# Performance work log

Measured on AMD Instinct MI355X. Metric: run time of the kernel, lower is better.

Reference implementation:

```python
import jax, jax.numpy as jnp
import numpy as np

N, E = 50000, 800000
IN_DIM, HID, OUT_DIM, H = 64, 64, 32, 2
NEG_SLOPE = 0.2
TEMP = 1.0
EPS = 1e-20


def gat_conv(x, edge_index, W, att_src, att_dst, bias):
    """PyG GATConv (concat=True, add_self_loops=True, eval mode so dropout off)."""
    n = x.shape[0]
    C = att_src.shape[1]
    # add self-loops (PyG default)
    loops = jnp.arange(n, dtype=edge_index.dtype)
    src = jnp.concatenate([edge_index[0], loops])
    dst = jnp.concatenate([edge_index[1], loops])
    xl = (x @ W).reshape(n, H, C)                      # [N,H,C]
    a_src = (xl * att_src[None]).sum(-1)               # [N,H]
    a_dst = (xl * att_dst[None]).sum(-1)               # [N,H]
    alpha = jax.nn.leaky_relu(a_src[src] + a_dst[dst], NEG_SLOPE)  # [E',H]
    amax = jax.ops.segment_max(alpha, dst, num_segments=n)
    alpha = jnp.exp(alpha - amax[dst])
    denom = jax.ops.segment_sum(alpha, dst, num_segments=n)
    alpha = alpha / (denom[dst] + 1e-16)
    msg = xl[src] * alpha[..., None]                   # [E',H,C]
    out = jax.ops.segment_sum(msg, dst, num_segments=n)
    return out.reshape(n, H * C) + bias


def setup_inputs() -> dict:
    key = jax.random.key(0)
    ks = jax.random.split(key, 18)
    s = 0.05
    inp = {
        'x': jax.random.normal(ks[0], (N, IN_DIM), jnp.float32),
        'edge_index': jax.random.randint(ks[1], (2, E), 0, N, jnp.int64
                                         if jax.config.jax_enable_x64 else jnp.int32).astype(jnp.int32),
        'W0': jax.random.normal(ks[2], (IN_DIM, H * HID)) * s,
        'att_src0': jax.random.normal(ks[3], (H, HID)) * s,
        'att_dst0': jax.random.normal(ks[4], (H, HID)) * s,
        'bias0': jax.random.normal(ks[5], (H * HID,)) * s,
        'fcw0': jax.random.normal(ks[6], (H * HID, HID)) * s,
        'fcb0': jax.random.normal(ks[7], (HID,)) * s,
        'W1': jax.random.normal(ks[8], (HID, H * HID)) * s,
        'att_src1': jax.random.normal(ks[9], (H, HID)) * s,
        'att_dst1': jax.random.normal(ks[10], (H, HID)) * s,
        'bias1': jax.random.normal(ks[11], (H * HID,)) * s,
        'fcw1': jax.random.normal(ks[12], (H * HID, HID)) * s,
        'fcb1': jax.random.normal(ks[13], (HID,)) * s,
        'out_w': jax.random.normal(ks[14], (HID, OUT_DIM)) * s,
        'out_b': jax.random.normal(ks[15], (OUT_DIM,)) * s,
        'gumbel_u': jax.random.uniform(ks[16], (N, OUT_DIM), jnp.float32),
    }
    return inp


def reference(x, edge_index, W0, att_src0, att_dst0, bias0, fcw0, fcb0,
              W1, att_src1, att_dst1, bias1, fcw1, fcb1, out_w, out_b, gumbel_u):
    h = gat_conv(x, edge_index, W0, att_src0, att_dst0, bias0)
    h = jax.nn.elu(h) @ fcw0 + fcb0
    h = gat_conv(h, edge_index, W1, att_src1, att_dst1, bias1)
    h = jax.nn.elu(h) @ fcw1 + fcb1
    logits = h @ out_w + out_b
    g = -jnp.log(-jnp.log(gumbel_u + EPS) + EPS)
    return jax.nn.softmax((logits + g) / TEMP, axis=-1)
```

## Files before the change

### kernel.cpp

```cpp
#include <hip/hip_runtime.h>
#include <hip/hip_fp16.h>
#include <math.h>

#define HEADS 2
#define FDIM 128
#define INDIM 64
#define ODIM 32
#define NEG_SLOPE 0.2f
#define BSH 7
#define BW  128
#define NBLK 128

typedef _Float16 f16x8 __attribute__((ext_vector_type(8)));
typedef float f32x4 __attribute__((ext_vector_type(4)));
union H8 { uint4 u; f16x8 v; __half2 h2[4]; };
union H4 { uint2 u; __half2 h2[2]; };

__device__ __forceinline__ float elu1(float v) { return v > 0.f ? v : __expf(v) - 1.f; }

#define MFMA16(a, b, c) __builtin_amdgcn_mfma_f32_16x16x32_f16((a), (b), (c), 0, 0, 0)

__global__ __launch_bounds__(256) void k_hist2(const int* __restrict__ ei, int E_,
                                               int* __restrict__ cnt, int nb, int epb) {
    __shared__ int h[512];
    int t = threadIdx.x, blk = blockIdx.x;
    for (int i = t; i < nb; i += 256) h[i] = 0;
    __syncthreads();
    int e0 = blk * epb, e1 = min(E_, e0 + epb);
    for (int e = e0 + t; e < e1; e += 256)
        atomicAdd(&h[ei[E_ + e] >> BSH], 1);
    __syncthreads();
    for (int i = t; i < nb; i += 256) cnt[i * NBLK + blk] = h[i];
}

__global__ __launch_bounds__(512) void k_scanb(const int* __restrict__ cnt,
                                               int* __restrict__ bstart,
                                               int* __restrict__ base, int nb, int E_) {
    __shared__ int sc[512];
    int t = threadIdx.x;
    int tot = 0;
    if (t < nb)
        for (int k = 0; k < NBLK; ++k) tot += cnt[t * NBLK + k];
    sc[t] = tot;
    __syncthreads();
    for (int o = 1; o < 512; o <<= 1) {
        int add = (t >= o) ? sc[t - o] : 0;
        __syncthreads();
        sc[t] += add;
        __syncthreads();
    }
    int ex = sc[t] - tot;
    if (t < nb) {
        bstart[t] = ex;
        int run = ex;
        for (int k = 0; k < NBLK; ++k) {
            base[t * NBLK + k] = run;
            run += cnt[t * NBLK + k];
        }
    }
    if (t == 0) bstart[nb] = E_;
}

__global__ __launch_bounds__(256) void k_scatter2(const int* __restrict__ ei, int E_,
                                                  const int* __restrict__ base,
                                                  unsigned* __restrict__ ebuf,
                                                  int nb, int epb) {
    __shared__ int pcur[512];
    int t = threadIdx.x, blk = blockIdx.x;
    for (int i = t; i < nb; i += 256) pcur[i] = base[i * NBLK + blk];
    __syncthreads();
    int e0 = blk * epb, e1 = min(E_, e0 + epb);
    for (int e = e0 + t; e < e1; e += 256) {
        int s = ei[e], d = ei[E_ + e];
        int slot = atomicAdd(&pcur[d >> BSH], 1);
        ebuf[slot] = ((unsigned)(d & (BW - 1)) << 25) | (unsigned)s;
    }
}

__global__ __launch_bounds__(256) void k_bfill(const unsigned* __restrict__ ebuf,
                                               const int* __restrict__ bstart,
                                               int* __restrict__ offs,
                                               int* __restrict__ csr_src, int n) {
    __shared__ int hist[BW], sc[BW], pcur[BW];
    int b = blockIdx.x;
    int t = threadIdx.x;
    int base_ = bstart[b];
    int cnt = bstart[b + 1] - base_;
    int d0 = b << BSH;
    if (t < BW) hist[t] = 0;
    __syncthreads();
    for (int i = t; i < cnt; i += 256)
        atomicAdd(&hist[ebuf[base_ + i] >> 25], 1);
    __syncthreads();
    int v = (t < BW) ? hist[t] : 0;
    if (t < BW) sc[t] = v;
    __syncthreads();
    for (int o = 1; o < BW; o <<= 1) {
        int add = (t < BW && t >= o) ? sc[t - o] : 0;
        __syncthreads();
        if (t < BW) sc[t] += add;
        __syncthreads();
    }
    if (t < BW) {
        int abspos = base_ + sc[t] - v;
        pcur[t] = abspos;
        if (d0 + t < n) offs[d0 + t] = abspos;
    }
    __syncthreads();
    for (int i = t; i < cnt; i += 256) {
        unsigned u = ebuf[base_ + i];
        int slot = atomicAdd(&pcur[u >> 25], 1);
        csr_src[slot] = (int)(u & 0x1FFFFFFu);
    }
}

__global__ __launch_bounds__(128) void k_fuse_w(
    const float* __restrict__ W0,
    const float* __restrict__ fcw0, const float* __restrict__ fcb0, const float* __restrict__ W1,
    const float* __restrict__ fcw1, const float* __restrict__ fcb1,
    const float* __restrict__ out_w, const float* __restrict__ out_b,
    __half* __restrict__ W0T, __half* __restrict__ WfT, float* __restrict__ bf,
    __half* __restrict__ WfoT, float* __restrict__ bfo)
{
    int b = blockIdx.x, c = threadIdx.x;
    if (b < 128) {
        float acc = 0.f;
        for (int j = 0; j < 64; ++j) acc = fmaf(fcw0[b * 64 + j], W1[j * 128 + c], acc);
        WfT[c * 128 + b] = __float2half(acc);
    } else if (b == 128) {
        float acc = 0.f;
        for (int j = 0; j < 64; ++j) acc = fmaf(fcb0[j], W1[j * 128 + c], acc);
        bf[c] = acc;
    } else if (b < 257) {
        int k = b - 129;
        if (c < 32) {
            float acc = 0.f;
            for (int j = 0; j < 64; ++j) acc = fmaf(fcw1[k * 64 + j], out_w[j * 32 + c], acc);
            WfoT[c * 128 + k] = __float2half(acc);
        }
    } else if (b == 257) {
        if (c < 32) {
            float acc = 0.f;
            for (int j = 0; j < 64; ++j) acc = fmaf(fcb1[j], out_w[j * 32 + c], acc);
            bfo[c] = acc + out_b[c];
        }
    } else {
        int k = b - 258;
        W0T[c * 64 + k] = __float2half(W0[k * 128 + c]);
    }
}

__global__ __launch_bounds__(256, 2) void k_mm_att1(
    const float* __restrict__ x, const __half* __restrict__ w0t,
    const float* __restrict__ att_src, const float* __restrict__ att_dst,
    __half* __restrict__ xl, float* __restrict__ a_src, float* __restrict__ a_dst,
    int n, int ntiles, int nwaves)
{
    int lane = threadIdx.x & 63;
    int wid = blockIdx.x * 4 + (threadIdx.x >> 6);
    int m = lane & 15, q = lane >> 4;

    H8 A[8][2];
    #pragma unroll
    for (int nt = 0; nt < 8; ++nt)
        #pragma unroll
        for (int kt = 0; kt < 2; ++kt)
            A[nt][kt].u = *(const uint4*)(w0t + (size_t)(nt * 16 + m) * 64 + kt * 32 + q * 8);

    for (int t = wid; t < ntiles; t += nwaves) {
        int rb = t * 16;
        int row = rb + m; if (row >= n) row = n - 1;
        H8 B[2];
        #pragma unroll
        for (int kt = 0; kt < 2; ++kt) {
            const float4* p = (const float4*)(x + (size_t)row * 64 + kt * 32 + q * 8);
            float4 p0 = p[0], p1 = p[1];
            B[kt].h2[0] = __floats2half2_rn(p0.x, p0.y);
            B[kt].h2[1] = __floats2half2_rn(p0.z, p0.w);
            B[kt].h2[2] = __floats2half2_rn(p1.x, p1.y);
            B[kt].h2[3] = __floats2half2_rn(p1.z, p1.w);
        }
        f32x4 acc[8];
        #pragma unroll
        for (int nt = 0; nt < 8; ++nt) {
            acc[nt] = {0.f, 0.f, 0.f, 0.f};
            acc[nt] = MFMA16(A[nt][0].v, B[0].v, acc[nt]);
            acc[nt] = MFMA16(A[nt][1].v, B[1].v, acc[nt]);
        }
        float ps0 = 0.f, ps1 = 0.f, pd0 = 0.f, pd1 = 0.f;
        bool ok = (rb + m) < n;
        #pragma unroll
        for (int nt = 0; nt < 8; ++nt) {
            float4 asv = *(const float4*)(att_src + nt * 16 + q * 4);
            float4 adv = *(const float4*)(att_dst + nt * 16 + q * 4);
            f32x4 d = acc[nt];
            H4 pk;
            pk.h2[0] = __floats2half2_rn(d[0], d[1]);
            pk.h2[1] = __floats2half2_rn(d[2], d[3]);
            if (ok) *(uint2*)(xl + (size_t)(rb + m) * 128 + nt * 16 + q * 4) = pk.u;
            float cs = d[0] * asv.x + d[1] * asv.y + d[2] * asv.z + d[3] * asv.w;
            float cd = d[0] * adv.x + d[1] * adv.y + d[2] * adv.z + d[3] * adv.w;
            if (nt < 4) { ps0 += cs; pd0 += cd; } else { ps1 += cs; pd1 += cd; }
        }
        ps0 += __shfl_xor(ps0, 16, 64); ps0 += __shfl_xor(ps0, 32, 64);
        ps1 += __shfl_xor(ps1, 16, 64); ps1 += __shfl_xor(ps1, 32, 64);
        pd0 += __shfl_xor(pd0, 16, 64); pd0 += __shfl_xor(pd0, 32, 64);
        pd1 += __shfl_xor(pd1, 16, 64); pd1 += __shfl_xor(pd1, 32, 64);
        if (lane < 16 && ok) {
            *(float2*)(a_src + (size_t)(rb + m) * 2) = make_float2(ps0, ps1);
            *(float2*)(a_dst + (size_t)(rb + m) * 2) = make_float2(pd0, pd1);
        }
    }
}

__global__ __launch_bounds__(256, 2) void k_mm_att2(
    const float* __restrict__ g, const __half* __restrict__ wft, const float* __restrict__ bf,
    const float* __restrict__ att_src, const float* __restrict__ att_dst,
    __half* __restrict__ xl, float* __restrict__ a_src, float* __restrict__ a_dst,
    int n, int ntiles, int nwaves)
{
    int lane = threadIdx.x & 63;
    int wid = blockIdx.x * 4 + (threadIdx.x >> 6);
    int m = lane & 15, q = lane >> 4;

    H8 A[8][4];
    #pragma unroll
    for (int nt = 0; nt < 8; ++nt)
        #pragma unroll
        for (int kt = 0; kt < 4; ++kt)
            A[nt][kt].u = *(const uint4*)(wft + (size_t)(nt * 16 + m) * 128 + kt * 32 + q * 8);

    for (int t = wid; t < ntiles; t += nwaves) {
        int rb = t * 16;
        int row = rb + m; if (row >= n) row = n - 1;
        H8 B[4];
        #pragma unroll
        for (int kt = 0; kt < 4; ++kt) {
            const float4* p = (const float4*)(g + (size_t)row * 128 + kt * 32 + q * 8);
            float4 p0 = p[0], p1 = p[1];
            B[kt].h2[0] = __floats2half2_rn(elu1(p0.x), elu1(p0.y));
            B[kt].h2[1] = __floats2half2_rn(elu1(p0.z), elu1(p0.w));
            B[kt].h2[2] = __floats2half2_rn(elu1(p1.x), elu1(p1.y));
            B[kt].h2[3] = __floats2half2_rn(elu1(p1.z), elu1(p1.w));
        }
        f32x4 acc[8];
        #pragma unroll
        for (int nt = 0; nt < 8; ++nt) {
            acc[nt] = {0.f, 0.f, 0.f, 0.f};
            #pragma unroll
            for (int kt = 0; kt < 4; ++kt)
                acc[nt] = MFMA16(A[nt][kt].v, B[kt].v, acc[nt]);
        }
        float ps0 = 0.f, ps1 = 0.f, pd0 = 0.f, pd1 = 0.f;
        bool ok = (rb + m) < n;
        #pragma unroll
        for (int nt = 0; nt < 8; ++nt) {
            float4 bfv = *(const float4*)(bf + nt * 16 + q * 4);
            float4 asv = *(const float4*)(att_src + nt * 16 + q * 4);
            float4 adv = *(const float4*)(att_dst + nt * 16 + q * 4);
            f32x4 d = acc[nt];
            d[0] += bfv.x; d[1] += bfv.y; d[2] += bfv.z; d[3] += bfv.w;
            H4 pk;
            pk.h2[0] = __floats2half2_rn(d[0], d[1]);
            pk.h2[1] = __floats2half2_rn(d[2], d[3]);
            if (ok) *(uint2*)(xl + (size_t)(rb + m) * 128 + nt * 16 + q * 4) = pk.u;
            float cs = d[0] * asv.x + d[1] * asv.y + d[2] * asv.z + d[3] * asv.w;
            float cd = d[0] * adv.x + d[1] * adv.y + d[2] * adv.z + d[3] * adv.w;
            if (nt < 4) { ps0 += cs; pd0 += cd; } else { ps1 += cs; pd1 += cd; }
        }
        ps0 += __shfl_xor(ps0, 16, 64); ps0 += __shfl_xor(ps0, 32, 64);
        ps1 += __shfl_xor(ps1, 16, 64); ps1 += __shfl_xor(ps1, 32, 64);
        pd0 += __shfl_xor(pd0, 16, 64); pd0 += __shfl_xor(pd0, 32, 64);
        pd1 += __shfl_xor(pd1, 16, 64); pd1 += __shfl_xor(pd1, 32, 64);
        if (lane < 16 && ok) {
            *(float2*)(a_src + (size_t)(rb + m) * 2) = make_float2(ps0, ps1);
            *(float2*)(a_dst + (size_t)(rb + m) * 2) = make_float2(pd0, pd1);
        }
    }
}

__global__ __launch_bounds__(256, 4) void k_gather(
    const int* __restrict__ offs, const int* __restrict__ csr_src, int E_,
    const __half* __restrict__ xl, const float* __restrict__ a_src,
    const float* __restrict__ a_dst, const float* __restrict__ bias,
    float* __restrict__ out, int n)
{
    int t = threadIdx.x;
    int lane = t & 63;
    int d = blockIdx.x * 4 + (t >> 6);
    if (d >= n) return;
    int eh = lane >> 4;
    int cq = lane & 15;
    int h = cq >> 3;
    float ad = a_dst[d * 2 + h];
    const float4* bp = (const float4*)(bias + cq * 8);
    float4 b0 = bp[0], b1 = bp[1];
    int start = offs[d];
    int end = (d + 1 < n) ? offs[d + 1] : E_;
    float acc[8] = {0.f, 0.f, 0.f, 0.f, 0.f, 0.f, 0.f, 0.f};
    float den = 0.f;
    for (int j0 = start; j0 < end; j0 += 4) {
        int j = j0 + eh;
        bool valid = j < end;
        int s = valid ? csr_src[j] : d;
        float a = a_src[s * 2 + h] + ad;
        a = (a >= 0.f) ? a : NEG_SLOPE * a;
        float w = valid ? __expf(a) : 0.f;
        float4 raw = *(const float4*)(xl + (size_t)s * 128 + cq * 8);
        __half2* hp = (__half2*)&raw;
        float2 f0 = __half22float2(hp[0]);
        float2 f1 = __half22float2(hp[1]);
        float2 f2 = __half22float2(hp[2]);
        float2 f3 = __half22float2(hp[3]);
        acc[0] = fmaf(w, f0.x, acc[0]); acc[1] = fmaf(w, f0.y, acc[1]);
        acc[2] = fmaf(w, f1.x, acc[2]); acc[3] = fmaf(w, f1.y, acc[3]);
        acc[4] = fmaf(w, f2.x, acc[4]); acc[5] = fmaf(w, f2.y, acc[5]);
        acc[6] = fmaf(w, f3.x, acc[6]); acc[7] = fmaf(w, f3.y, acc[7]);
        den += w;
    }
    if (eh == 0) {
        float a = a_src[d * 2 + h] + ad;
        a = (a >= 0.f) ? a : NEG_SLOPE * a;
        float w = __expf(a);
        float4 raw = *(const float4*)(xl + (size_t)d * 128 + cq * 8);
        __half2* hp = (__half2*)&raw;
        float2 f0 = __half22float2(hp[0]);
        float2 f1 = __half22float2(hp[1]);
        float2 f2 = __half22float2(hp[2]);
        float2 f3 = __half22float2(hp[3]);
        acc[0] = fmaf(w, f0.x, acc[0]); acc[1] = fmaf(w, f0.y, acc[1]);
        acc[2] = fmaf(w, f1.x, acc[2]); acc[3] = fmaf(w, f1.y, acc[3]);
        acc[4] = fmaf(w, f2.x, acc[4]); acc[5] = fmaf(w, f2.y, acc[5]);
        acc[6] = fmaf(w, f3.x, acc[6]); acc[7] = fmaf(w, f3.y, acc[7]);
        den += w;
    }
    #pragma unroll
    for (int i = 0; i < 8; ++i) {
        acc[i] += __shfl_xor(acc[i], 16, 64);
        acc[i] += __shfl_xor(acc[i], 32, 64);
    }
    den += __shfl_xor(den, 16, 64);
    den += __shfl_xor(den, 32, 64);
    if (eh == 0) {
        float inv = 1.f / (den + 1e-16f);
        float4 o0 = make_float4(fmaf(acc[0], inv, b0.x), fmaf(acc[1], inv, b0.y),
                                fmaf(acc[2], inv, b0.z), fmaf(acc[3], inv, b0.w));
        float4 o1 = make_float4(fmaf(acc[4], inv, b1.x), fmaf(acc[5], inv, b1.y),
                                fmaf(acc[6], inv, b1.z), fmaf(acc[7], inv, b1.w));
        float4* op = (float4*)(out + (size_t)d * 128 + cq * 8);
        op[0] = o0; op[1] = o1;
    }
}

__global__ __launch_bounds__(256, 2) void k_mm_final(
    const float* __restrict__ g, const __half* __restrict__ wfot, const float* __restrict__ bfo,
    const float* __restrict__ gu, float* __restrict__ out, int n, int ntiles, int nwaves)
{
    int lane = threadIdx.x & 63;
    int wid = blockIdx.x * 4 + (threadIdx.x >> 6);
    int m = lane & 15, q = lane >> 4;

    H8 A[2][4];
    #pragma unroll
    for (int nt = 0; nt < 2; ++nt)
        #pragma unroll
        for (int kt = 0; kt < 4; ++kt)
            A[nt][kt].u = *(const uint4*)(wfot + (size_t)(nt * 16 + m) * 128 + kt * 32 + q * 8);

    for (int t = wid; t < ntiles; t += nwaves) {
        int rb = t * 16;
        int row = rb + m; if (row >= n) row = n - 1;
        H8 B[4];
        #pragma unroll
        for (int kt = 0; kt < 4; ++kt) {
            const float4* p = (const float4*)(g + (size_t)row * 128 + kt * 32 + q * 8);
            float4 p0 = p[0], p1 = p[1];
            B[kt].h2[0] = __floats2half2_rn(elu1(p0.x), elu1(p0.y));
            B[kt].h2[1] = __floats2half2_rn(elu1(p0.z), elu1(p0.w));
            B[kt].h2[2] = __floats2half2_rn(elu1(p1.x), elu1(p1.y));
            B[kt].h2[3] = __floats2half2_rn(elu1(p1.z), elu1(p1.w));
        }
        f32x4 acc[2];
        #pragma unroll
        for (int nt = 0; nt < 2; ++nt) {
            acc[nt] = {0.f, 0.f, 0.f, 0.f};
            #pragma unroll
            for (int kt = 0; kt < 4; ++kt)
                acc[nt] = MFMA16(A[nt][kt].v, B[kt].v, acc[nt]);
        }
        float z[8];
        #pragma unroll
        for (int nt = 0; nt < 2; ++nt) {
            float4 bv = *(const float4*)(bfo + nt * 16 + q * 4);
            float4 uv = *(const float4*)(gu + (size_t)row * 32 + nt * 16 + q * 4);
            z[nt * 4 + 0] = acc[nt][0] + bv.x - __logf(-__logf(uv.x + 1e-20f) + 1e-20f);
            z[nt * 4 + 1] = acc[nt][1] + bv.y - __logf(-__logf(uv.y + 1e-20f) + 1e-20f);
            z[nt * 4 + 2] = acc[nt][2] + bv.z - __logf(-__logf(uv.z + 1e-20f) + 1e-20f);
            z[nt * 4 + 3] = acc[nt][3] + bv.w - __logf(-__logf(uv.w + 1e-20f) + 1e-20f);
        }
        float mx = z[0];
        #pragma unroll
        for (int i = 1; i < 8; ++i) mx = fmaxf(mx, z[i]);
        mx = fmaxf(mx, __shfl_xor(mx, 16, 64));
        mx = fmaxf(mx, __shfl_xor(mx, 32, 64));
        float sum = 0.f;
        #pragma unroll
        for (int i = 0; i < 8; ++i) { z[i] = __expf(z[i] - mx); sum += z[i]; }
        sum += __shfl_xor(sum, 16, 64);
        sum += __shfl_xor(sum, 32, 64);
        float inv = 1.f / sum;
        if (rb + m < n) {
            #pragma unroll
            for (int nt = 0; nt < 2; ++nt) {
                float4 o = make_float4(z[nt * 4 + 0] * inv, z[nt * 4 + 1] * inv,
                                       z[nt * 4 + 2] * inv, z[nt * 4 + 3] * inv);
                *(float4*)(out + (size_t)(rb + m) * 32 + nt * 16 + q * 4) = o;
            }
        }
    }
}

extern "C" void kernel_launch(void* const* d_in, const int* in_sizes, int n_in,
                              void* d_out, int out_size, void* d_ws, size_t ws_size,
                              hipStream_t stream) {
    const float* x        = (const float*)d_in[0];
    const int*   ei       = (const int*)  d_in[1];
    const float* W0       = (const float*)d_in[2];
    const float* att_src0 = (const float*)d_in[3];
    const float* att_dst0 = (const float*)d_in[4];
    const float* bias0    = (const float*)d_in[5];
    const float* fcw0     = (const float*)d_in[6];
    const float* fcb0     = (const float*)d_in[7];
    const float* W1       = (const float*)d_in[8];
    const float* att_src1 = (const float*)d_in[9];
    const float* att_dst1 = (const float*)d_in[10];
    const float* bias1    = (const float*)d_in[11];
    const float* fcw1     = (const float*)d_in[12];
    const float* fcb1     = (const float*)d_in[13];
    const float* out_w    = (const float*)d_in[14];
    const float* out_b    = (const float*)d_in[15];
    const float* gu       = (const float*)d_in[16];

    const int N_ = in_sizes[0] / INDIM;
    const int E_ = in_sizes[1] / 2;
    const int NB = (N_ + BW - 1) / BW;

    float* ws = (float*)d_ws;
    size_t off = 0;
    __half* xl  = (__half*)(ws + off); off += (size_t)N_ * 64;
    float* gat   = ws + off; off += (size_t)N_ * FDIM;
    float* a_src = ws + off; off += (size_t)N_ * HEADS;
    float* a_dst = ws + off; off += (size_t)N_ * HEADS;
    __half* W0T  = (__half*)(ws + off); off += 128 * 64 / 2;
    __half* WfT  = (__half*)(ws + off); off += 128 * 128 / 2;
    __half* WfoT = (__half*)(ws + off); off += 32 * 128 / 2;
    float* bf    = ws + off; off += 128;
    float* bfo   = ws + off; off += 32;
    int* cnt     = (int*)(ws + off); off += (size_t)NB * NBLK;
    int* base    = (int*)(ws + off); off += (size_t)NB * NBLK;
    int* bstart  = (int*)(ws + off); off += NB + 1;
    int* offs    = (int*)(ws + off); off += N_;
    int* csr_src = (int*)(ws + off); off += E_;
    unsigned* ebuf = (unsigned*)(ws + off); off += E_;

    const int B = 256;
    dim3 blk(B);
    int g_gath = (N_ + 3) / 4;
    int ntiles = (N_ + 15) / 16;
    int GMM    = 384;
    int nwaves = GMM * 4;
    int epb    = (E_ + NBLK - 1) / NBLK;

    k_hist2    <<<NBLK, blk, 0, stream>>>(ei, E_, cnt, NB, epb);
    k_scanb    <<<1, dim3(512), 0, stream>>>(cnt, bstart, base, NB, E_);
    k_scatter2 <<<NBLK, blk, 0, stream>>>(ei, E_, base, ebuf, NB, epb);
    k_bfill    <<<NB, blk, 0, stream>>>(ebuf, bstart, offs, csr_src, N_);
    k_fuse_w   <<<322, dim3(128), 0, stream>>>(W0, fcw0, fcb0, W1, fcw1, fcb1, out_w, out_b,
                                               W0T, WfT, bf, WfoT, bfo);

    k_mm_att1 <<<GMM,    blk, 0, stream>>>(x, W0T, att_src0, att_dst0, xl, a_src, a_dst,
                                           N_, ntiles, nwaves);
    k_gather  <<<g_gath, blk, 0, stream>>>(offs, csr_src, E_, xl, a_src, a_dst, bias0, gat, N_);

    k_mm_att2 <<<GMM,    blk, 0, stream>>>(gat, WfT, bf, att_src1, att_dst1, xl, a_src, a_dst,
                                           N_, ntiles, nwaves);
    k_gather  <<<g_gath, blk, 0, stream>>>(offs, csr_src, E_, xl, a_src, a_dst, bias1, gat, N_);

    k_mm_final <<<GMM,   blk, 0, stream>>>(gat, WfoT, bfo, gu, (float*)d_out, N_, ntiles, nwaves);
}
```

Baseline: 297.0 us.

## Store GAT aggregation output in fp16, unroll gather by two, transpose bucket counts

The intermediate GAT output buffer becomes fp16 instead of fp32. This halves the write traffic in the gather kernel and the read traffic in the two following matmul kernels, and adds an extra rounding step before the ELU. The gather loop now processes two edges per lane per iteration so that more independent loads are in flight. The histogram count and base arrays are switched to block-major layout so the per-block writes and reads are contiguous, while the scan kernel now reads them strided.

```diff
diff --git a/kernel.cpp b/kernel.cpp
--- a/kernel.cpp
+++ b/kernel.cpp
@@ -30,7 +30,7 @@
     for (int e = e0 + t; e < e1; e += 256)
         atomicAdd(&h[ei[E_ + e] >> BSH], 1);
     __syncthreads();
-    for (int i = t; i < nb; i += 256) cnt[i * NBLK + blk] = h[i];
+    for (int i = t; i < nb; i += 256) cnt[blk * nb + i] = h[i];
 }
 
 __global__ __launch_bounds__(512) void k_scanb(const int* __restrict__ cnt,
@@ -40,7 +40,7 @@
     int t = threadIdx.x;
     int tot = 0;
     if (t < nb)
-        for (int k = 0; k < NBLK; ++k) tot += cnt[t * NBLK + k];
+        for (int k = 0; k < NBLK; ++k) tot += cnt[k * nb + t];
     sc[t] = tot;
     __syncthreads();
     for (int o = 1; o < 512; o <<= 1) {
@@ -54,8 +54,8 @@
         bstart[t] = ex;
         int run = ex;
         for (int k = 0; k < NBLK; ++k) {
-            base[t * NBLK + k] = run;
-            run += cnt[t * NBLK + k];
+            base[k * nb + t] = run;
+            run += cnt[k * nb + t];
         }
     }
     if (t == 0) bstart[nb] = E_;
@@ -67,7 +67,7 @@
                                                   int nb, int epb) {
     __shared__ int pcur[512];
     int t = threadIdx.x, blk = blockIdx.x;
-    for (int i = t; i < nb; i += 256) pcur[i] = base[i * NBLK + blk];
+    for (int i = t; i < nb; i += 256) pcur[i] = base[blk * nb + i];
     __syncthreads();
     int e0 = blk * epb, e1 = min(E_, e0 + epb);
     for (int e = e0 + t; e < e1; e += 256) {
@@ -214,7 +214,7 @@
 }
 
 __global__ __launch_bounds__(256, 2) void k_mm_att2(
-    const float* __restrict__ g, const __half* __restrict__ wft, const float* __restrict__ bf,
+    const __half* __restrict__ g, const __half* __restrict__ wft, const float* __restrict__ bf,
     const float* __restrict__ att_src, const float* __restrict__ att_dst,
     __half* __restrict__ xl, float* __restrict__ a_src, float* __restrict__ a_dst,
     int n, int ntiles, int nwaves)
@@ -236,12 +236,13 @@
         H8 B[4];
         #pragma unroll
         for (int kt = 0; kt < 4; ++kt) {
-            const float4* p = (const float4*)(g + (size_t)row * 128 + kt * 32 + q * 8);
-            float4 p0 = p[0], p1 = p[1];
-            B[kt].h2[0] = __floats2half2_rn(elu1(p0.x), elu1(p0.y));
-            B[kt].h2[1] = __floats2half2_rn(elu1(p0.z), elu1(p0.w));
-            B[kt].h2[2] = __floats2half2_rn(elu1(p1.x), elu1(p1.y));
-            B[kt].h2[3] = __floats2half2_rn(elu1(p1.z), elu1(p1.w));
+            H8 raw;
+            raw.u = *(const uint4*)(g + (size_t)row * 128 + kt * 32 + q * 8);
+            #pragma unroll
+            for (int r = 0; r < 4; ++r) {
+                float2 f = __half22float2(raw.h2[r]);
+                B[kt].h2[r] = __floats2half2_rn(elu1(f.x), elu1(f.y));
+            }
         }
         f32x4 acc[8];
         #pragma unroll
@@ -283,7 +284,7 @@
     const int* __restrict__ offs, const int* __restrict__ csr_src, int E_,
     const __half* __restrict__ xl, const float* __restrict__ a_src,
     const float* __restrict__ a_dst, const float* __restrict__ bias,
-    float* __restrict__ out, int n)
+    __half* __restrict__ out, int n)
 {
     int t = threadIdx.x;
     int lane = t & 63;
@@ -299,24 +300,31 @@
     int end = (d + 1 < n) ? offs[d + 1] : E_;
     float acc[8] = {0.f, 0.f, 0.f, 0.f, 0.f, 0.f, 0.f, 0.f};
     float den = 0.f;
-    for (int j0 = start; j0 < end; j0 += 4) {
-        int j = j0 + eh;
-        bool valid = j < end;
-        int s = valid ? csr_src[j] : d;
-        float a = a_src[s * 2 + h] + ad;
-        a = (a >= 0.f) ? a : NEG_SLOPE * a;
-        float w = valid ? __expf(a) : 0.f;
-        float4 raw = *(const float4*)(xl + (size_t)s * 128 + cq * 8);
-        __half2* hp = (__half2*)&raw;
-        float2 f0 = __half22float2(hp[0]);
-        float2 f1 = __half22float2(hp[1]);
-        float2 f2 = __half22float2(hp[2]);
-        float2 f3 = __half22float2(hp[3]);
-        acc[0] = fmaf(w, f0.x, acc[0]); acc[1] = fmaf(w, f0.y, acc[1]);
-        acc[2] = fmaf(w, f1.x, acc[2]); acc[3] = fmaf(w, f1.y, acc[3]);
-        acc[4] = fmaf(w, f2.x, acc[4]); acc[5] = fmaf(w, f2.y, acc[5]);
-        acc[6] = fmaf(w, f3.x, acc[6]); acc[7] = fmaf(w, f3.y, acc[7]);
-        den += w;
+    for (int j0 = start; j0 < end; j0 += 8) {
+        int ja = j0 + eh, jb = j0 + 4 + eh;
+        bool va = ja < end, vb = jb < end;
+        int sa = va ? csr_src[ja] : d;
+        int sb = vb ? csr_src[jb] : d;
+        float4 ra = *(const float4*)(xl + (size_t)sa * 128 + cq * 8);
+        float4 rb = *(const float4*)(xl + (size_t)sb * 128 + cq * 8);
+        float aa = a_src[sa * 2 + h] + ad;
+        float ab = a_src[sb * 2 + h] + ad;
+        aa = (aa >= 0.f) ? aa : NEG_SLOPE * aa;
+        ab = (ab >= 0.f) ? ab : NEG_SLOPE * ab;
+        float wa = va ? __expf(aa) : 0.f;
+        float wb = vb ? __expf(ab) : 0.f;
+        __half2* ha = (__half2*)&ra;
+        __half2* hb = (__half2*)&rb;
+        #pragma unroll
+        for (int r = 0; r < 4; ++r) {
+            float2 fa = __half22float2(ha[r]);
+            float2 fb = __half22float2(hb[r]);
+            acc[2 * r]     = fmaf(wa, fa.x, acc[2 * r]);
+            acc[2 * r + 1] = fmaf(wa, fa.y, acc[2 * r + 1]);
+            acc[2 * r]     = fmaf(wb, fb.x, acc[2 * r]);
+            acc[2 * r + 1] = fmaf(wb, fb.y, acc[2 * r + 1]);
+        }
+        den += wa + wb;
     }
     if (eh == 0) {
         float a = a_src[d * 2 + h] + ad;
@@ -324,14 +332,12 @@
         float w = __expf(a);
         float4 raw = *(const float4*)(xl + (size_t)d * 128 + cq * 8);
         __half2* hp = (__half2*)&raw;
-        float2 f0 = __half22float2(hp[0]);
-        float2 f1 = __half22float2(hp[1]);
-        float2 f2 = __half22float2(hp[2]);
-        float2 f3 = __half22float2(hp[3]);
-        acc[0] = fmaf(w, f0.x, acc[0]); acc[1] = fmaf(w, f0.y, acc[1]);
-        acc[2] = fmaf(w, f1.x, acc[2]); acc[3] = fmaf(w, f1.y, acc[3]);
-        acc[4] = fmaf(w, f2.x, acc[4]); acc[5] = fmaf(w, f2.y, acc[5]);
-        acc[6] = fmaf(w, f3.x, acc[6]); acc[7] = fmaf(w, f3.y, acc[7]);
+        #pragma unroll
+        for (int r = 0; r < 4; ++r) {
+            float2 f = __half22float2(hp[r]);
+            acc[2 * r]     = fmaf(w, f.x, acc[2 * r]);
+            acc[2 * r + 1] = fmaf(w, f.y, acc[2 * r + 1]);
+        }
         den += w;
     }
     #pragma unroll
@@ -343,17 +349,17 @@
     den += __shfl_xor(den, 32, 64);
     if (eh == 0) {
         float inv = 1.f / (den + 1e-16f);
-        float4 o0 = make_float4(fmaf(acc[0], inv, b0.x), fmaf(acc[1], inv, b0.y),
-                                fmaf(acc[2], inv, b0.z), fmaf(acc[3], inv, b0.w));
-        float4 o1 = make_float4(fmaf(acc[4], inv, b1.x), fmaf(acc[5], inv, b1.y),
-                                fmaf(acc[6], inv, b1.z), fmaf(acc[7], inv, b1.w));
-        float4* op = (float4*)(out + (size_t)d * 128 + cq * 8);
-        op[0] = o0; op[1] = o1;
+        H8 pk;
+        pk.h2[0] = __floats2half2_rn(fmaf(acc[0], inv, b0.x), fmaf(acc[1], inv, b0.y));
+        pk.h2[1] = __floats2half2_rn(fmaf(acc[2], inv, b0.z), fmaf(acc[3], inv, b0.w));
+        pk.h2[2] = __floats2half2_rn(fmaf(acc[4], inv, b1.x), fmaf(acc[5], inv, b1.y));
+        pk.h2[3] = __floats2half2_rn(fmaf(acc[6], inv, b1.z), fmaf(acc[7], inv, b1.w));
+        *(uint4*)(out + (size_t)d * 128 + cq * 8) = pk.u;
     }
 }
 
 __global__ __launch_bounds__(256, 2) void k_mm_final(
-    const float* __restrict__ g, const __half* __restrict__ wfot, const float* __restrict__ bfo,
+    const __half* __restrict__ g, const __half* __restrict__ wfot, const float* __restrict__ bfo,
     const float* __restrict__ gu, float* __restrict__ out, int n, int ntiles, int nwaves)
 {
     int lane = threadIdx.x & 63;
@@ -373,12 +379,13 @@
         H8 B[4];
         #pragma unroll
         for (int kt = 0; kt < 4; ++kt) {
-            const float4* p = (const float4*)(g + (size_t)row * 128 + kt * 32 + q * 8);
-            float4 p0 = p[0], p1 = p[1];
-            B[kt].h2[0] = __floats2half2_rn(elu1(p0.x), elu1(p0.y));
-            B[kt].h2[1] = __floats2half2_rn(elu1(p0.z), elu1(p0.w));
-            B[kt].h2[2] = __floats2half2_rn(elu1(p1.x), elu1(p1.y));
-            B[kt].h2[3] = __floats2half2_rn(elu1(p1.z), elu1(p1.w));
+            H8 raw;
+            raw.u = *(const uint4*)(g + (size_t)row * 128 + kt * 32 + q * 8);
+            #pragma unroll
+            for (int r = 0; r < 4; ++r) {
+                float2 f = __half22float2(raw.h2[r]);
+                B[kt].h2[r] = __floats2half2_rn(elu1(f.x), elu1(f.y));
+            }
         }
         f32x4 acc[2];
         #pragma unroll
@@ -448,7 +455,7 @@
     float* ws = (float*)d_ws;
     size_t off = 0;
     __half* xl  = (__half*)(ws + off); off += (size_t)N_ * 64;
-    float* gat   = ws + off; off += (size_t)N_ * FDIM;
+    __half* gat = (__half*)(ws + off); off += (size_t)N_ * 64;
     float* a_src = ws + off; off += (size_t)N_ * HEADS;
     float* a_dst = ws + off; off += (size_t)N_ * HEADS;
     __half* W0T  = (__half*)(ws + off); off += 128 * 64 / 2;
```

Measured after the change: 257.0 us. -13.5%, faster.
